# Kernel tuning notes

Measured on AMD Instinct MI355X. Metric: run time of the kernel, lower is better.

The kernel has to match this reference:

```python
import jax, jax.numpy as jnp
import numpy as np

FT_IN = 40960   # HalfKP-style feature space
FFT_IN = 640    # factorized piece-square features
FT_OUT = 256


def setup_inputs() -> dict:
    key = jax.random.key(0)
    ks = jax.random.split(key, 10)
    B, A = 16384, 30  # batch, active features per board
    inp = {
        "stm_idx": jax.random.randint(ks[0], (B, A), 0, FT_IN, dtype=jnp.int32),
        "nstm_idx": jax.random.randint(ks[1], (B, A), 0, FT_IN, dtype=jnp.int32),
        "f_stm_idx": jax.random.randint(ks[2], (B, A), 0, FFT_IN, dtype=jnp.int32),
        "f_nstm_idx": jax.random.randint(ks[3], (B, A), 0, FFT_IN, dtype=jnp.int32),
        # learned parameters (glorot-ish scale)
        "ft_w": jax.random.normal(ks[4], (FT_IN, FT_OUT), jnp.float32) * 0.01,
        "ft_b": jax.random.normal(ks[5], (FT_OUT,), jnp.float32) * 0.01,
        "fft_w": jax.random.normal(ks[6], (FFT_IN, FT_OUT), jnp.float32) * 0.05,
        "fft_b": jax.random.normal(ks[7], (FT_OUT,), jnp.float32) * 0.01,
        "out_w": jax.random.normal(ks[8], (2 * FT_OUT, 1), jnp.float32) * 0.05,
        "out_b": jax.random.normal(ks[9], (1,), jnp.float32) * 0.01,
    }
    return inp


def _accumulate(w, b, idx):
    # sparse one-hot board @ kernel + bias == gather rows and sum over active features
    return jnp.take(w, idx, axis=0).sum(axis=1) + b  # [B, FT_OUT]


def reference(stm_idx, nstm_idx, f_stm_idx, f_nstm_idx,
              ft_w, ft_b, fft_w, fft_b, out_w, out_b):
    stm = _accumulate(ft_w, ft_b, stm_idx)        # [B, 256]
    nstm = _accumulate(ft_w, ft_b, nstm_idx)      # [B, 256]
    f_stm = _accumulate(fft_w, fft_b, f_stm_idx)  # [B, 256]
    f_nstm = _accumulate(fft_w, fft_b, f_nstm_idx)
    merge = jnp.concatenate((stm, nstm), axis=1) + jnp.concatenate((f_stm, f_nstm), axis=1)
    h = jnp.clip(merge, 0.0, 1.0)                 # ReLU(max_value=1.0)
    return jax.nn.sigmoid(h @ out_w + out_b)      # [B, 1]
```

## Files before the change

### kernel.cpp

```cpp
#include <hip/hip_runtime.h>
#include <math.h>

#define FT_IN  40960
#define FFT_IN 640
#define FT_OUT 256
#define NA     30
#define NSLICE 8
#define BPB    64
#define PD     6

typedef _Float16 h2 __attribute__((ext_vector_type(2)));
typedef unsigned u32x4 __attribute__((ext_vector_type(4)));

__device__ __forceinline__ h2 u2h2(unsigned u) {
    union { unsigned u; h2 h; } c; c.u = u; return c.h;
}
__device__ __forceinline__ unsigned pkh(float a, float b) {
    union { h2 h; unsigned u; } c; c.h = h2{(_Float16)a, (_Float16)b}; return c.u;
}

__device__ __forceinline__ void conv_block(const float* __restrict__ src,
                                           unsigned* __restrict__ dst,
                                           int nrows, int bid, int tid)
{
    int t = bid * 256 + tid;
    int total = nrows * 32;
    if (t >= total) return;
    int r = t >> 5, g = t & 31;
    int s = g >> 2, d = g & 3;
    const float4* sp = (const float4*)(src + (size_t)r * FT_OUT + g * 8);
    float4 v0 = sp[0], v1 = sp[1];
    uint4 u;
    u.x = pkh(v0.x, v0.y); u.y = pkh(v0.z, v0.w);
    u.z = pkh(v1.x, v1.y); u.w = pkh(v1.z, v1.w);
    ((uint4*)dst)[((size_t)s * nrows + r) * 4 + d] = u;
}

__global__ __launch_bounds__(256) void prep(
    const float* __restrict__ ft_w, const float* __restrict__ fft_w,
    const int* __restrict__ stm, const int* __restrict__ nstm,
    const int* __restrict__ fstm, const int* __restrict__ fnstm,
    unsigned* __restrict__ ft_o, unsigned* __restrict__ fft_o,
    ushort4* __restrict__ pidx, int n_boards, int nb_ft, int nb_fft)
{
    int bid = blockIdx.x;
    if (bid < nb_ft) {
        conv_block(ft_w, ft_o, FT_IN, bid, threadIdx.x);
    } else if (bid < nb_ft + nb_fft) {
        conv_block(fft_w, fft_o, FFT_IN, bid - nb_ft, threadIdx.x);
    } else {
        int t = (bid - nb_ft - nb_fft) * 256 + (int)threadIdx.x;
        int total = n_boards * NA;
        if (t < total) {
            int board = t / NA, a = t - board * NA;
            ushort4 v;
            v.x = (unsigned short)stm[t];  v.y = (unsigned short)nstm[t];
            v.z = (unsigned short)fstm[t]; v.w = (unsigned short)fnstm[t];
            pidx[(size_t)a * n_boards + board] = v;
        }
    }
}

__global__ __launch_bounds__(256) void nnue_gather(
    const uint2* __restrict__ pidx,
    const char* __restrict__ ft, const char* __restrict__ fft,
    const float* __restrict__ ft_b, const float* __restrict__ fft_b,
    const float* __restrict__ out_w, float* __restrict__ partial, int n_boards)
{
    __shared__ uint2 lidx[NA][BPB];
    __shared__ u32x4 lfft[FFT_IN * 4];
    const int slice = blockIdx.x & (NSLICE - 1);
    const int group = blockIdx.x >> 3;
    const int tid = (int)threadIdx.x;

    {
        for (int i = tid; i < NA * BPB; i += 256) {
            int a = i >> 6, b = i & 63;
            int bd = group * BPB + b;
            uint2 v;
            if (bd < n_boards) v = pidx[(size_t)a * n_boards + bd];
            else { v.x = 0; v.y = 0; }
            lidx[a][b] = v;
        }
        const u32x4* fsrc = (const u32x4*)(fft + (size_t)slice * FFT_IN * 64);
        for (int i = tid; i < FFT_IN * 4; i += 256) {
            int r = i >> 2, c = i & 3;
            lfft[(r << 2) + (c ^ ((r >> 1) & 3))] = fsrc[i];
        }
    }
    __syncthreads();

    const int sub = tid >> 2, ql = tid & 3;
    int board = group * BPB + sub;
    const bool active = board < n_boards;
    const unsigned qlo = (unsigned)(ql << 4);
    const unsigned long long ftbase =
        (unsigned long long)(ft + (size_t)slice * FT_IN * 64);
    const int col = slice * 32 + ql * 8;

    h2 z = h2{(_Float16)0.f, (_Float16)0.f};
    h2 a0[4] = {z, z, z, z};
    h2 a1[4] = {z, z, z, z};

    u32x4 fs[PD], fn[PD];
    #pragma unroll
    for (int a = 0; a < PD; ++a) {
        uint2 iv = lidx[a][sub];
        unsigned o0 = ((iv.x & 0xFFFFu) << 6) + qlo;
        unsigned o1 = ((iv.x >> 16) << 6) + qlo;
        asm volatile("global_load_dwordx4 %0, %1, %2"
                     : "=v"(fs[a]) : "v"(o0), "s"(ftbase));
        asm volatile("global_load_dwordx4 %0, %1, %2"
                     : "=v"(fn[a]) : "v"(o1), "s"(ftbase));
    }

#define STEP(A)                                                              \
    {                                                                        \
        uint2 ivA = lidx[(A)][sub];                                          \
        unsigned rz = ivA.y & 0xFFFFu, rw = ivA.y >> 16;                     \
        u32x4 g0 = lfft[(rz << 2) + (ql ^ ((rz >> 1) & 3))];                 \
        u32x4 g1 = lfft[(rw << 2) + (ql ^ ((rw >> 1) & 3))];                 \
        asm volatile("s_waitcnt vmcnt(%2)"                                   \
                     : "+v"(fs[(A) % PD]), "+v"(fn[(A) % PD])                \
                     : "n"(2 * ((NA - (A)) < PD ? (NA - (A)) : PD) - 2));    \
        u32x4 u0 = fs[(A) % PD], u1 = fn[(A) % PD];                          \
        a0[0] += u2h2(u0.x); a0[1] += u2h2(u0.y);                            \
        a0[2] += u2h2(u0.z); a0[3] += u2h2(u0.w);                            \
        a1[0] += u2h2(u1.x); a1[1] += u2h2(u1.y);                            \
        a1[2] += u2h2(u1.z); a1[3] += u2h2(u1.w);                            \
        a0[0] += u2h2(g0.x); a0[1] += u2h2(g0.y);                            \
        a0[2] += u2h2(g0.z); a0[3] += u2h2(g0.w);                            \
        a1[0] += u2h2(g1.x); a1[1] += u2h2(g1.y);                            \
        a1[2] += u2h2(g1.z); a1[3] += u2h2(g1.w);                            \
        if ((A) + PD < NA) {                                                 \
            uint2 ivB = lidx[(A) + PD][sub];                                 \
            unsigned o0 = ((ivB.x & 0xFFFFu) << 6) + qlo;                    \
            unsigned o1 = ((ivB.x >> 16) << 6) + qlo;                        \
            asm volatile("global_load_dwordx4 %0, %1, %2"                    \
                         : "=v"(fs[(A) % PD]) : "v"(o0), "s"(ftbase));       \
            asm volatile("global_load_dwordx4 %0, %1, %2"                    \
                         : "=v"(fn[(A) % PD]) : "v"(o1), "s"(ftbase));       \
        }                                                                    \
    }

    STEP(0)  STEP(1)  STEP(2)  STEP(3)  STEP(4)  STEP(5)
    STEP(6)  STEP(7)  STEP(8)  STEP(9)  STEP(10) STEP(11)
    STEP(12) STEP(13) STEP(14) STEP(15) STEP(16) STEP(17)
    STEP(18) STEP(19) STEP(20) STEP(21) STEP(22) STEP(23)
    STEP(24) STEP(25) STEP(26) STEP(27) STEP(28) STEP(29)
#undef STEP

    float h0[8], h1[8];
    #pragma unroll
    for (int i = 0; i < 4; ++i) {
        h0[2*i] = (float)a0[i].x; h0[2*i+1] = (float)a0[i].y;
        h1[2*i] = (float)a1[i].x; h1[2*i+1] = (float)a1[i].y;
    }
    const float4* bfp = (const float4*)(ft_b  + col);
    const float4* bgp = (const float4*)(fft_b + col);
    float4 bf0 = bfp[0], bf1 = bfp[1], bg0 = bgp[0], bg1 = bgp[1];
    float bias[8] = {bf0.x+bg0.x, bf0.y+bg0.y, bf0.z+bg0.z, bf0.w+bg0.w,
                     bf1.x+bg1.x, bf1.y+bg1.y, bf1.z+bg1.z, bf1.w+bg1.w};
    const float4* w0p = (const float4*)(out_w + col);
    const float4* w1p = (const float4*)(out_w + FT_OUT + col);
    float4 w00 = w0p[0], w01 = w0p[1], w10 = w1p[0], w11 = w1p[1];
    float w0[8] = {w00.x, w00.y, w00.z, w00.w, w01.x, w01.y, w01.z, w01.w};
    float w1[8] = {w10.x, w10.y, w10.z, w10.w, w11.x, w11.y, w11.z, w11.w};

    float p = 0.f;
    #pragma unroll
    for (int i = 0; i < 8; ++i) {
        p += fminf(fmaxf(h0[i] + bias[i], 0.f), 1.f) * w0[i];
        p += fminf(fmaxf(h1[i] + bias[i], 0.f), 1.f) * w1[i];
    }
    p += __shfl_xor(p, 1, 64);
    p += __shfl_xor(p, 2, 64);
    if (active && ql == 0) partial[(size_t)slice * n_boards + board] = p;
}

__global__ __launch_bounds__(256) void nnue_final(
    const float* __restrict__ partial, const float* __restrict__ out_b,
    float* __restrict__ out, int n)
{
    int b = blockIdx.x * blockDim.x + threadIdx.x;
    if (b >= n) return;
    float zv = out_b[0];
    #pragma unroll
    for (int s = 0; s < NSLICE; ++s) zv += partial[(size_t)s * n + b];
    out[b] = 1.0f / (1.0f + expf(-zv));
}

__global__ __launch_bounds__(256) void nnue_fwd_direct(
    const int* __restrict__ stm_idx, const int* __restrict__ nstm_idx,
    const int* __restrict__ f_stm_idx, const int* __restrict__ f_nstm_idx,
    const float* __restrict__ ft_w, const float* __restrict__ ft_b,
    const float* __restrict__ fft_w, const float* __restrict__ fft_b,
    const float* __restrict__ out_w, const float* __restrict__ out_b,
    float* __restrict__ out, int n_boards)
{
    const int board = (int)((blockIdx.x * blockDim.x + threadIdx.x) >> 6);
    const int lane  = (int)(threadIdx.x & 63);
    if (board >= n_boards) return;
    const int col = lane << 2;
    const float4 ftb  = *(const float4*)(ft_b  + col);
    const float4 fftb = *(const float4*)(fft_b + col);
    float a0x = ftb.x + fftb.x, a0y = ftb.y + fftb.y,
          a0z = ftb.z + fftb.z, a0w = ftb.w + fftb.w;
    float a1x = a0x, a1y = a0y, a1z = a0z, a1w = a0w;
    const int* si  = stm_idx    + (size_t)board * NA;
    const int* ni  = nstm_idx   + (size_t)board * NA;
    const int* fsi = f_stm_idx  + (size_t)board * NA;
    const int* fni = f_nstm_idx + (size_t)board * NA;
    #pragma unroll 5
    for (int a = 0; a < NA; ++a) {
        const float4 r0 = *(const float4*)(ft_w  + (size_t)si[a]  * FT_OUT + col);
        const float4 r1 = *(const float4*)(ft_w  + (size_t)ni[a]  * FT_OUT + col);
        const float4 r2 = *(const float4*)(fft_w + (size_t)fsi[a] * FT_OUT + col);
        const float4 r3 = *(const float4*)(fft_w + (size_t)fni[a] * FT_OUT + col);
        a0x += r0.x + r2.x; a0y += r0.y + r2.y; a0z += r0.z + r2.z; a0w += r0.w + r2.w;
        a1x += r1.x + r3.x; a1y += r1.y + r3.y; a1z += r1.z + r3.z; a1w += r1.w + r3.w;
    }
    a0x = fminf(fmaxf(a0x, 0.f), 1.f); a0y = fminf(fmaxf(a0y, 0.f), 1.f);
    a0z = fminf(fmaxf(a0z, 0.f), 1.f); a0w = fminf(fmaxf(a0w, 0.f), 1.f);
    a1x = fminf(fmaxf(a1x, 0.f), 1.f); a1y = fminf(fmaxf(a1y, 0.f), 1.f);
    a1z = fminf(fmaxf(a1z, 0.f), 1.f); a1w = fminf(fmaxf(a1w, 0.f), 1.f);
    const float4 w0 = *(const float4*)(out_w + col);
    const float4 w1 = *(const float4*)(out_w + FT_OUT + col);
    float p = a0x * w0.x + a0y * w0.y + a0z * w0.z + a0w * w0.w
            + a1x * w1.x + a1y * w1.y + a1z * w1.z + a1w * w1.w;
    #pragma unroll
    for (int off = 32; off > 0; off >>= 1) p += __shfl_down(p, off, 64);
    if (lane == 0) out[board] = 1.0f / (1.0f + expf(-(p + out_b[0])));
}

extern "C" void kernel_launch(void* const* d_in, const int* in_sizes, int n_in,
                              void* d_out, int out_size, void* d_ws, size_t ws_size,
                              hipStream_t stream) {
    const int*   stm_idx    = (const int*)d_in[0];
    const int*   nstm_idx   = (const int*)d_in[1];
    const int*   f_stm_idx  = (const int*)d_in[2];
    const int*   f_nstm_idx = (const int*)d_in[3];
    const float* ft_w  = (const float*)d_in[4];
    const float* ft_b  = (const float*)d_in[5];
    const float* fft_w = (const float*)d_in[6];
    const float* fft_b = (const float*)d_in[7];
    const float* out_w = (const float*)d_in[8];
    const float* out_b = (const float*)d_in[9];
    float* out = (float*)d_out;

    const int n_boards = in_sizes[0] / NA;

    const size_t ft_bytes   = (size_t)FT_IN  * FT_OUT * 2;
    const size_t fft_bytes  = (size_t)FFT_IN * FT_OUT * 2;
    const size_t pidx_bytes = (size_t)n_boards * NA * sizeof(ushort4);
    const size_t part_bytes = (size_t)n_boards * NSLICE * sizeof(float);
    const size_t need = ft_bytes + fft_bytes + pidx_bytes + part_bytes;

    if (ws_size < need) {
        const int grid = (n_boards + 3) / 4;
        nnue_fwd_direct<<<grid, 256, 0, stream>>>(stm_idx, nstm_idx, f_stm_idx, f_nstm_idx,
                                                  ft_w, ft_b, fft_w, fft_b, out_w, out_b,
                                                  out, n_boards);
        return;
    }

    char* wsp = (char*)d_ws;
    unsigned* ws_ft   = (unsigned*)wsp;            wsp += ft_bytes;
    unsigned* ws_fft  = (unsigned*)wsp;            wsp += fft_bytes;
    ushort4*  ws_pidx = (ushort4*)wsp;             wsp += pidx_bytes;
    float*    ws_part = (float*)wsp;

    {
        const int nb_ft   = FT_IN  * 32 / 256;
        const int nb_fft  = FFT_IN * 32 / 256;
        const int nb_pack = (n_boards * NA + 255) / 256;
        prep<<<nb_ft + nb_fft + nb_pack, 256, 0, stream>>>(
            ft_w, fft_w, stm_idx, nstm_idx, f_stm_idx, f_nstm_idx,
            ws_ft, ws_fft, ws_pidx, n_boards, nb_ft, nb_fft);
    }
    {
        int groups = (n_boards + BPB - 1) / BPB;
        nnue_gather<<<groups * NSLICE, 256, 0, stream>>>(
            (const uint2*)ws_pidx, (const char*)ws_ft, (const char*)ws_fft,
            ft_b, fft_b, out_w, ws_part, n_boards);
    }
    {
        nnue_final<<<(n_boards + 255) / 256, 256, 0, stream>>>(ws_part, out_b, out, n_boards);
    }
}
```

Before: 157.7 us.

## Split active-feature loop across two thread halves per board, 512-thread blocks

Each board is now handled by 8 threads instead of 4. Two half-groups each accumulate 15 of the 30 active features, and their fp16 partial sums are combined with a lane-xor shuffle. The block size doubles to 512 so the dependent gather chain per thread is halved and more loads are in flight, at the cost of extra shuffles and more threads per block. The LDS swizzle for the factorized table is replaced by row padding to avoid bank conflicts.

```diff
diff --git a/kernel.cpp b/kernel.cpp
--- a/kernel.cpp
+++ b/kernel.cpp
@@ -5,6 +5,7 @@
 #define FFT_IN 640
 #define FT_OUT 256
 #define NA     30
+#define NH     15
 #define NSLICE 8
 #define BPB    64
 #define PD     6
@@ -17,6 +18,11 @@
 }
 __device__ __forceinline__ unsigned pkh(float a, float b) {
     union { h2 h; unsigned u; } c; c.h = h2{(_Float16)a, (_Float16)b}; return c.u;
+}
+__device__ __forceinline__ h2 foldx4(h2 v) {
+    union { h2 h; int i; } c; c.h = v;
+    c.i = __shfl_xor(c.i, 4, 64);
+    return v + c.h;
 }
 
 __device__ __forceinline__ void conv_block(const float* __restrict__ src,
@@ -61,36 +67,37 @@
     }
 }
 
-__global__ __launch_bounds__(256) void nnue_gather(
+__global__ __launch_bounds__(512, 4) void nnue_gather(
     const uint2* __restrict__ pidx,
     const char* __restrict__ ft, const char* __restrict__ fft,
     const float* __restrict__ ft_b, const float* __restrict__ fft_b,
     const float* __restrict__ out_w, float* __restrict__ partial, int n_boards)
 {
-    __shared__ uint2 lidx[NA][BPB];
-    __shared__ u32x4 lfft[FFT_IN * 4];
+    __shared__ uint2 lidx[NA * BPB];
+    __shared__ u32x4 lfft[FFT_IN * 4 + FFT_IN / 2];
     const int slice = blockIdx.x & (NSLICE - 1);
     const int group = blockIdx.x >> 3;
     const int tid = (int)threadIdx.x;
 
-    {
-        for (int i = tid; i < NA * BPB; i += 256) {
-            int a = i >> 6, b = i & 63;
-            int bd = group * BPB + b;
-            uint2 v;
-            if (bd < n_boards) v = pidx[(size_t)a * n_boards + bd];
-            else { v.x = 0; v.y = 0; }
-            lidx[a][b] = v;
+    for (int i = tid; i < NA * BPB; i += 512) {
+        int b = i & 63;
+        int bd = group * BPB + b;
+        uint2 v; v.x = 0u; v.y = 0u;
+        if (bd < n_boards) v = pidx[(size_t)(i >> 6) * n_boards + bd];
+        lidx[i] = v;
+    }
+    {
+        const u32x4* fsrc = (const u32x4*)(fft + (size_t)slice * FFT_IN * 64);
+        for (int i = tid; i < FFT_IN * 4; i += 512) {
+            int r = i >> 2, c = i & 3;
+            lfft[(r << 2) + (r >> 1) + c] = fsrc[i];
         }
-        const u32x4* fsrc = (const u32x4*)(fft + (size_t)slice * FFT_IN * 64);
-        for (int i = tid; i < FFT_IN * 4; i += 256) {
-            int r = i >> 2, c = i & 3;
-            lfft[(r << 2) + (c ^ ((r >> 1) & 3))] = fsrc[i];
-        }
     }
     __syncthreads();
 
-    const int sub = tid >> 2, ql = tid & 3;
+    const int sub  = tid >> 3;
+    const int ql   = tid & 3;
+    const int hoff = ((tid >> 2) & 1) * NH;
     int board = group * BPB + sub;
     const bool active = board < n_boards;
     const unsigned qlo = (unsigned)(ql << 4);
@@ -105,7 +112,7 @@
     u32x4 fs[PD], fn[PD];
     #pragma unroll
     for (int a = 0; a < PD; ++a) {
-        uint2 iv = lidx[a][sub];
+        uint2 iv = lidx[(hoff + a) * BPB + sub];
         unsigned o0 = ((iv.x & 0xFFFFu) << 6) + qlo;
         unsigned o1 = ((iv.x >> 16) << 6) + qlo;
         asm volatile("global_load_dwordx4 %0, %1, %2"
@@ -116,13 +123,13 @@
 
 #define STEP(A)                                                              \
     {                                                                        \
-        uint2 ivA = lidx[(A)][sub];                                          \
+        uint2 ivA = lidx[(hoff + (A)) * BPB + sub];                          \
         unsigned rz = ivA.y & 0xFFFFu, rw = ivA.y >> 16;                     \
-        u32x4 g0 = lfft[(rz << 2) + (ql ^ ((rz >> 1) & 3))];                 \
-        u32x4 g1 = lfft[(rw << 2) + (ql ^ ((rw >> 1) & 3))];                 \
+        u32x4 g0 = lfft[(rz << 2) + (rz >> 1) + ql];                         \
+        u32x4 g1 = lfft[(rw << 2) + (rw >> 1) + ql];                         \
         asm volatile("s_waitcnt vmcnt(%2)"                                   \
                      : "+v"(fs[(A) % PD]), "+v"(fn[(A) % PD])                \
-                     : "n"(2 * ((NA - (A)) < PD ? (NA - (A)) : PD) - 2));    \
+                     : "n"(2 * ((NH - (A)) < PD ? (NH - (A)) : PD) - 2));    \
         u32x4 u0 = fs[(A) % PD], u1 = fn[(A) % PD];                          \
         a0[0] += u2h2(u0.x); a0[1] += u2h2(u0.y);                            \
         a0[2] += u2h2(u0.z); a0[3] += u2h2(u0.w);                            \
@@ -132,8 +139,8 @@
         a0[2] += u2h2(g0.z); a0[3] += u2h2(g0.w);                            \
         a1[0] += u2h2(g1.x); a1[1] += u2h2(g1.y);                            \
         a1[2] += u2h2(g1.z); a1[3] += u2h2(g1.w);                            \
-        if ((A) + PD < NA) {                                                 \
-            uint2 ivB = lidx[(A) + PD][sub];                                 \
+        if ((A) + PD < NH) {                                                 \
+            uint2 ivB = lidx[(hoff + (A) + PD) * BPB + sub];                 \
             unsigned o0 = ((ivB.x & 0xFFFFu) << 6) + qlo;                    \
             unsigned o1 = ((ivB.x >> 16) << 6) + qlo;                        \
             asm volatile("global_load_dwordx4 %0, %1, %2"                    \
@@ -143,12 +150,13 @@
         }                                                                    \
     }
 
-    STEP(0)  STEP(1)  STEP(2)  STEP(3)  STEP(4)  STEP(5)
-    STEP(6)  STEP(7)  STEP(8)  STEP(9)  STEP(10) STEP(11)
-    STEP(12) STEP(13) STEP(14) STEP(15) STEP(16) STEP(17)
-    STEP(18) STEP(19) STEP(20) STEP(21) STEP(22) STEP(23)
-    STEP(24) STEP(25) STEP(26) STEP(27) STEP(28) STEP(29)
+    STEP(0)  STEP(1)  STEP(2)  STEP(3)  STEP(4)
+    STEP(5)  STEP(6)  STEP(7)  STEP(8)  STEP(9)
+    STEP(10) STEP(11) STEP(12) STEP(13) STEP(14)
 #undef STEP
+
+    #pragma unroll
+    for (int j = 0; j < 4; ++j) { a0[j] = foldx4(a0[j]); a1[j] = foldx4(a1[j]); }
 
     float h0[8], h1[8];
     #pragma unroll
@@ -175,7 +183,8 @@
     }
     p += __shfl_xor(p, 1, 64);
     p += __shfl_xor(p, 2, 64);
-    if (active && ql == 0) partial[(size_t)slice * n_boards + board] = p;
+    if (active && (tid & 7) == 0)
+        partial[(size_t)slice * n_boards + board] = p;
 }
 
 __global__ __launch_bounds__(256) void nnue_final(
@@ -280,7 +289,7 @@
     }
     {
         int groups = (n_boards + BPB - 1) / BPB;
-        nnue_gather<<<groups * NSLICE, 256, 0, stream>>>(
+        nnue_gather<<<groups * NSLICE, 512, 0, stream>>>(
             (const uint2*)ws_pidx, (const char*)ws_ft, (const char*)ws_fft,
             ft_b, fft_b, out_w, ws_part, n_boards);
     }
```

After: 151.6 us. 3.9% less time.
